# Optimization experiments

Hardware: AMD Instinct MI355X
Metric: run time of the kernel (lower is better)

## Reference

```python
import jax, jax.numpy as jnp
import numpy as np

B, S, D, DH = 4, 2048, 1024, 64


def setup_inputs() -> dict:
    key = jax.random.key(0)
    ks = jax.random.split(key, 7)
    x = jax.random.normal(ks[0], (B, S, D), dtype=jnp.float32)
    def w(k):
        return jax.random.normal(k, (D, DH), dtype=jnp.float32) / np.sqrt(D).astype(np.float32)
    return {
        'x': x,
        'w_q_u': w(ks[1]), 'w_k_u': w(ks[2]), 'w_v_u': w(ks[3]),
        'w_q_c': w(ks[4]), 'w_k_c': w(ks[5]), 'w_v_c': w(ks[6]),
    }


def reference(x, w_q_u, w_k_u, w_v_u, w_q_c, w_k_c, w_v_c):
    b, n, _ = x.shape
    scale = w_q_u.shape[-1] ** -0.5
    # projections (LinearNoBias -> plain matmul)
    Q_u = x @ w_q_u
    K_u = x @ w_k_u
    V_u = x @ w_v_u
    Q_c = x @ w_q_c
    K_c = x @ w_k_c
    V_c = x @ w_v_c

    i = jnp.arange(n)
    causal = i[:, None] >= i[None, :]        # True where j <= i (binary causal / keep for S_c)
    lookahead = i[:, None] < i[None, :]      # True where j > i (allowed in sigmoid term)

    # term1: [b, n, n], zeroed above the diagonal via binary causal mask
    term1 = jnp.einsum('bid,bjd->bij', Q_c, V_u) * scale * causal.astype(x.dtype)

    # sigmoid gate: lookahead mask adds -inf on/below the diagonal -> sigmoid = 0 there
    logits_u = jnp.einsum('bid,bjd->bij', Q_u, K_u) * scale
    sigmoid_term = jax.nn.sigmoid(jnp.where(lookahead, logits_u, -jnp.inf))

    # nested n^3 matmul: S_u[b,i,k] = sum_j term1[b,i,j] * sigmoid_term[b,k,j]
    S_u = jnp.einsum('bij,bkj->bik', term1, sigmoid_term)

    S_c = jnp.where(causal, jnp.einsum('bid,bjd->bij', Q_c, K_c) * scale, -jnp.inf)

    attn = jax.nn.softmax(S_c - jax.nn.silu(S_u), axis=-1)
    return jnp.einsum('bij,bjd->bid', attn, V_c)
```

## Files before the change

### kernel.cpp

```cpp
#include <hip/hip_runtime.h>
#include <hip/hip_bf16.h>

typedef short bf16x8 __attribute__((ext_vector_type(8)));
typedef float f32x4  __attribute__((ext_vector_type(4)));
typedef _Float16 f16x8 __attribute__((ext_vector_type(8)));

#define MFMA16(a,b,c)  __builtin_amdgcn_mfma_f32_16x16x32_bf16((a),(b),(c),0,0,0)
#define MFMAF16(a,b,c) __builtin_amdgcn_mfma_f32_16x16x32_f16((a),(b),(c),0,0,0)

#define GLDS16(g,l) __builtin_amdgcn_global_load_lds( \
    (const __attribute__((address_space(1))) void*)(g), \
    (__attribute__((address_space(3))) void*)(l), 16, 0, 0)

__device__ __forceinline__ short f2bf(float f){
  union { float f; unsigned u; } v; v.f = f;
  unsigned r = v.u + 0x7fffu + ((v.u >> 16) & 1u);
  return (short)(r >> 16);
}
__device__ __forceinline__ float bf2f(short h){
  union { unsigned u; float f; } v; v.u = ((unsigned)(unsigned short)h) << 16;
  return v.f;
}
__device__ __forceinline__ void split8v(f32x4 a, f32x4 b, bf16x8& h, bf16x8& l){
  float t[8] = {a[0],a[1],a[2],a[3],b[0],b[1],b[2],b[3]};
  #pragma unroll
  for (int e = 0; e < 8; ++e){
    short hs = f2bf(t[e]);
    h[e] = hs;
    l[e] = f2bf(t[e] - bf2f(hs));
  }
}

__global__ void k_wt(const float* w0, const float* w1, const float* w2,
                     const float* w3, const float* w4, const float* w5,
                     unsigned short* __restrict__ wth, unsigned short* __restrict__ wtl){
  int p = blockIdx.y;
  const float* wp = p==0?w0:p==1?w1:p==2?w2:p==3?w3:p==4?w4:w5;
  int idx = blockIdx.x*256 + threadIdx.x;
  int n = idx >> 10, k = idx & 1023;
  float v = wp[k*64 + n];
  short hs = f2bf(v);
  wth[(size_t)p*65536 + n*1024 + k] = (unsigned short)hs;
  wtl[(size_t)p*65536 + n*1024 + k] = (unsigned short)f2bf(v - bf2f(hs));
}

__global__ void k_xsplit(const float* __restrict__ x,
                         unsigned short* __restrict__ xh, unsigned short* __restrict__ xl){
  size_t i = ((size_t)blockIdx.x*256 + threadIdx.x)*8;
  f32x4 a = *(const f32x4*)(x + i);
  f32x4 b = *(const f32x4*)(x + i + 4);
  bf16x8 h, l;
  split8v(a, b, h, l);
  *(bf16x8*)(xh + i) = h;
  *(bf16x8*)(xl + i) = l;
}

__global__ __launch_bounds__(256) void k_proj(
    const unsigned short* __restrict__ xh, const unsigned short* __restrict__ xl,
    const unsigned short* __restrict__ wth, const unsigned short* __restrict__ wtl,
    float* __restrict__ proj,
    unsigned short* __restrict__ projh, unsigned short* __restrict__ projl){
  __shared__ __align__(16) char sm[49152];
  int blk = blockIdx.x;
  int rb = blk/3, pg = blk - rb*3;
  int tid = threadIdx.x, w = tid >> 6, lane = tid & 63;
  int lm = lane & 15, quad = lane >> 4;
  int srow = lane >> 3, scg = (lane & 7) ^ srow;
  const char* xhg = (const char*)xh;
  const char* xlg = (const char*)xl;
  const char* w0h = (const char*)wth + (size_t)(pg*2  )*131072;
  const char* w0l = (const char*)wtl + (size_t)(pg*2  )*131072;
  const char* w1h = (const char*)wth + (size_t)(pg*2+1)*131072;
  const char* w1l = (const char*)wtl + (size_t)(pg*2+1)*131072;
  f32x4 acc[2][4] = {};
  for (int k0 = 0; k0 < 1024; k0 += 64){
    __syncthreads();
    size_t cb = (size_t)k0*2 + scg*16;
    #pragma unroll
    for (int i2 = 0; i2 < 2; ++i2){
      int i = w*2 + i2;
      size_t gx = (size_t)(rb*64 + i*8 + srow)*2048 + cb;
      size_t gw = (size_t)(i*8 + srow)*2048 + cb;
      GLDS16(xhg + gx, sm +         i*1024);
      GLDS16(xlg + gx, sm +  8192 + i*1024);
      GLDS16(w0h + gw, sm + 16384 + i*1024);
      GLDS16(w0l + gw, sm + 24576 + i*1024);
      GLDS16(w1h + gw, sm + 32768 + i*1024);
      GLDS16(w1l + gw, sm + 40960 + i*1024);
    }
    __syncthreads();
    #pragma unroll
    for (int ks = 0; ks < 2; ++ks){
      int ra = w*16 + lm;
      int offa = ra*128 + (((ks*4+quad) ^ (ra&7))*16);
      bf16x8 ah = *(const bf16x8*)(sm + offa);
      bf16x8 al = *(const bf16x8*)(sm + 8192 + offa);
      #pragma unroll
      for (int sub = 0; sub < 2; ++sub){
        #pragma unroll
        for (int n = 0; n < 4; ++n){
          int r = n*16 + lm;
          int off = r*128 + (((ks*4+quad) ^ (r&7))*16);
          bf16x8 bh = *(const bf16x8*)(sm + 16384 + sub*16384 + off);
          bf16x8 bl = *(const bf16x8*)(sm + 24576 + sub*16384 + off);
          acc[sub][n] = MFMA16(ah, bh, acc[sub][n]);
          acc[sub][n] = MFMA16(ah, bl, acc[sub][n]);
          acc[sub][n] = MFMA16(al, bh, acc[sub][n]);
        }
      }
    }
  }
  #pragma unroll
  for (int sub = 0; sub < 2; ++sub){
    int p = pg*2 + sub;
    if (p == 2 || p == 5){
      float* op = proj + (size_t)(p == 5 ? 1 : 0)*524288;
      #pragma unroll
      for (int n = 0; n < 4; ++n)
        #pragma unroll
        for (int e = 0; e < 4; ++e){
          int r = rb*64 + w*16 + quad*4 + e;
          op[(size_t)r*64 + n*16 + lm] = acc[sub][n][e];
        }
    }
    if (p != 5){
      unsigned short* oph = projh + (size_t)p*524288;
      unsigned short* opl = projl + (size_t)p*524288;
      #pragma unroll
      for (int n = 0; n < 4; ++n)
        #pragma unroll
        for (int e = 0; e < 4; ++e){
          int r = rb*64 + w*16 + quad*4 + e;
          float f = acc[sub][n][e];
          short hs = f2bf(f);
          oph[(size_t)r*64 + n*16 + lm] = (unsigned short)hs;
          opl[(size_t)r*64 + n*16 + lm] = (unsigned short)f2bf(f - bf2f(hs));
        }
    }
  }
}

__global__ void k_vt(const float* __restrict__ proj, _Float16* __restrict__ vct,
                     _Float16* __restrict__ vuth, _Float16* __restrict__ vutl){
  __shared__ float T[64][65];
  int b = blockIdx.y, stg = blockIdx.x;
  bool isVu = stg >= 32;
  int st = stg & 31;
  int tid = threadIdx.x;
  const float* src = proj + (isVu ? 0 : 524288) + (size_t)b*131072;
  int sloc = tid >> 2, cp = (tid & 3)*16;
  #pragma unroll
  for (int j = 0; j < 4; ++j){
    f32x4 v = *(const f32x4*)(src + (size_t)(st*64 + sloc)*64 + cp + j*4);
    #pragma unroll
    for (int e = 0; e < 4; ++e) T[sloc][cp + j*4 + e] = v[e];
  }
  __syncthreads();
  int d = tid >> 2, sp = (tid & 3)*16;
  size_t o = (size_t)b*131072 + (size_t)d*2048 + st*64 + sp;
  if (!isVu){
    f16x8 h0, h1;
    #pragma unroll
    for (int j = 0; j < 8; ++j) h0[j] = (_Float16)T[sp + j][d];
    #pragma unroll
    for (int j = 0; j < 8; ++j) h1[j] = (_Float16)T[sp + 8 + j][d];
    *(f16x8*)(vct + o) = h0; *(f16x8*)(vct + o + 8) = h1;
  } else {
    f16x8 h0, h1, l0, l1;
    #pragma unroll
    for (int j = 0; j < 8; ++j){
      float f = T[sp + j][d];
      _Float16 h = (_Float16)f;
      h0[j] = h; l0[j] = (_Float16)(f - (float)h);
    }
    #pragma unroll
    for (int j = 0; j < 8; ++j){
      float f = T[sp + 8 + j][d];
      _Float16 h = (_Float16)f;
      h1[j] = h; l1[j] = (_Float16)(f - (float)h);
    }
    *(f16x8*)(vuth + o) = h0; *(f16x8*)(vuth + o + 8) = h1;
    *(f16x8*)(vutl + o) = l0; *(f16x8*)(vutl + o + 8) = l1;
  }
}

__global__ __launch_bounds__(256,2) void k_p2(
    const unsigned short* __restrict__ ph, const unsigned short* __restrict__ pl,
    _Float16* __restrict__ sg, _Float16* __restrict__ t1d){
  __shared__ __align__(16) char sm[65536];
  int b = blockIdx.y;
  int t = blockIdx.x;
  bool isSig = t < 136;
  int a = 0, bb = 0;
  if (isSig){
    #pragma unroll 1
    for (int aa = 0; aa < 16; ++aa){
      int c = 16 - aa;
      if (t < c){ a = aa; bb = aa + t; break; }
      t -= c;
    }
  } else {
    a = bb = t - 136;
  }
  int pa = isSig ? 0 : 3;
  int pb = isSig ? 1 : 2;
  const char* Ahg = (const char*)ph + (size_t)pa*1048576;
  const char* Alg = (const char*)pl + (size_t)pa*1048576;
  const char* Bhg = (const char*)ph + (size_t)pb*1048576;
  const char* Blg = (const char*)pl + (size_t)pb*1048576;
  int tid = threadIdx.x, w = tid >> 6, lane = tid & 63;
  int lm = lane & 15, quad = lane >> 4;
  int srow = lane >> 3, scg = (lane & 7) ^ srow;
  int wm = (w & 1)*64, wn = (w >> 1)*64;
  #pragma unroll
  for (int i2 = 0; i2 < 4; ++i2){
    int i = w*4 + i2;
    int rl = i*8 + srow;
    size_t ga = (size_t)(b*2048 + a*128  + rl)*128 + scg*16;
    size_t gb = (size_t)(b*2048 + bb*128 + rl)*128 + scg*16;
    GLDS16(Ahg + ga, sm +         i*1024);
    GLDS16(Alg + ga, sm + 16384 + i*1024);
    GLDS16(Bhg + gb, sm + 32768 + i*1024);
    GLDS16(Blg + gb, sm + 49152 + i*1024);
  }
  __syncthreads();
  f32x4 acc[4][4] = {};
  #pragma unroll
  for (int ks = 0; ks < 2; ++ks){
    bf16x8 bh[4], bl[4];
    #pragma unroll
    for (int n = 0; n < 4; ++n){
      int r = wn + n*16 + lm;
      int off = r*128 + (((ks*4+quad) ^ (r&7))*16);
      bh[n] = *(const bf16x8*)(sm + 32768 + off);
      bl[n] = *(const bf16x8*)(sm + 49152 + off);
    }
    #pragma unroll
    for (int m = 0; m < 4; ++m){
      int r = wm + m*16 + lm;
      int off = r*128 + (((ks*4+quad) ^ (r&7))*16);
      bf16x8 ah = *(const bf16x8*)(sm + off);
      bf16x8 al = *(const bf16x8*)(sm + 16384 + off);
      #pragma unroll
      for (int n = 0; n < 4; ++n){
        acc[m][n] = MFMA16(ah, bh[n], acc[m][n]);
        acc[m][n] = MFMA16(ah, bl[n], acc[m][n]);
        acc[m][n] = MFMA16(al, bh[n], acc[m][n]);
      }
    }
  }
  __syncthreads();
  _Float16* Tt = (_Float16*)sm;
  #pragma unroll
  for (int m = 0; m < 4; ++m){
    #pragma unroll
    for (int n = 0; n < 4; ++n){
      #pragma unroll
      for (int e = 0; e < 4; ++e){
        int il = wm + m*16 + quad*4 + e;
        int jl = wn + n*16 + lm;
        int gi = a*128 + il, gj = bb*128 + jl;
        float v = acc[m][n][e];
        float outv;
        if (isSig) outv = (gj >  gi) ? (1.0f/(1.0f + __expf(-v*0.125f))) : 0.0f;
        else       outv = (gj <= gi) ? v : 0.0f;
        Tt[il*128 + jl] = (_Float16)outv;
      }
    }
  }
  __syncthreads();
  char* outp = isSig
    ? (char*)(sg + (size_t)b*4194304 + (size_t)(a*128)*2048 + bb*128)
    : (char*)t1d + (size_t)(b*16 + a)*32768;
  size_t rstride = isSig ? 4096 : 256;
  #pragma unroll
  for (int r = 0; r < 8; ++r){
    int lrow = w*32 + r*4 + (lane >> 4);
    int c16 = lane & 15;
    f32x4 vv = *(const f32x4*)(sm + lrow*256 + c16*16);
    *(f32x4*)(outp + (size_t)lrow*rstride + c16*16) = vv;
  }
}

__global__ __launch_bounds__(256) void k_w(
    const _Float16* __restrict__ sg,
    const _Float16* __restrict__ vuth, const _Float16* __restrict__ vutl,
    float* __restrict__ W){
  int p = blockIdx.x, b = blockIdx.y;
  int c = 0, ck = 0;
  #pragma unroll 1
  for (int aa = 0; aa < 16; ++aa){
    if (p < aa + 1){ c = aa; ck = p; break; }
    p -= aa + 1;
  }
  int pidx = blockIdx.x;
  int tid = threadIdx.x, w = tid >> 6, lane = tid & 63;
  int lm = lane & 15, quad = lane >> 4;
  int wm = (w & 1)*64, wn = (w >> 1)*32;
  const char* sgb = (const char*)sg + (size_t)b*8388608;
  f32x4 acc[4][2] = {};
  #pragma unroll
  for (int ks = 0; ks < 4; ++ks){
    f16x8 bh[2], bl[2];
    #pragma unroll
    for (int n = 0; n < 2; ++n){
      int d = wn + n*16 + lm;
      size_t jo = ((size_t)(b*64 + d)*2048 + c*128 + ks*32 + quad*8)*2;
      bh[n] = *(const f16x8*)((const char*)vuth + jo);
      bl[n] = *(const f16x8*)((const char*)vutl + jo);
    }
    #pragma unroll
    for (int m = 0; m < 4; ++m){
      int k = ck*128 + wm + m*16 + lm;
      f16x8 af = *(const f16x8*)(sgb + ((size_t)k*2048 + c*128 + ks*32 + quad*8)*2);
      #pragma unroll
      for (int n = 0; n < 2; ++n){
        acc[m][n] = MFMAF16(af, bh[n], acc[m][n]);
        acc[m][n] = MFMAF16(af, bl[n], acc[m][n]);
      }
    }
  }
  float* Wp = W + (size_t)(b*136 + pidx)*8192;
  #pragma unroll
  for (int m = 0; m < 4; ++m)
    #pragma unroll
    for (int n = 0; n < 2; ++n)
      #pragma unroll
      for (int e = 0; e < 4; ++e){
        int r = wm + m*16 + quad*4 + e;
        int col = wn + n*16 + lm;
        Wp[r*64 + col] = acc[m][n][e];
      }
}

__global__ __launch_bounds__(256) void k_scan(const float* __restrict__ W,
    unsigned short* __restrict__ Ph, unsigned short* __restrict__ Pl){
  int g = blockIdx.x, b = blockIdx.y;
  int ck = g >> 2, ksub = g & 3;
  if (ck >= 15) return;
  int tid = threadIdx.x;
  int rl = ksub*32 + (tid >> 3);
  int col = (tid & 7)*8;
  float acc[8] = {};
  #pragma unroll 1
  for (int c = ck; c < 15; ++c){
    const float* wt = W + (size_t)(b*136 + c*(c+1)/2 + ck)*8192 + rl*64 + col;
    f32x4 v0 = *(const f32x4*)wt;
    f32x4 v1 = *(const f32x4*)(wt + 4);
    #pragma unroll
    for (int e = 0; e < 4; ++e){ acc[e] += v0[e]; acc[4+e] += v1[e]; }
    size_t o = ((size_t)(b*16 + c + 1)*2048 + ck*128 + rl)*64 + col;
    bf16x8 h, l;
    #pragma unroll
    for (int e = 0; e < 8; ++e){
      short hs = f2bf(acc[e]);
      h[e] = hs;
      l[e] = f2bf(acc[e] - bf2f(hs));
    }
    *(bf16x8*)(Ph + o) = h;
    *(bf16x8*)(Pl + o) = l;
  }
}

__global__ __launch_bounds__(256,2) void k_p3(
    const unsigned short* __restrict__ ph, const unsigned short* __restrict__ pl,
    const _Float16* __restrict__ t1d, const _Float16* __restrict__ sg,
    const unsigned short* __restrict__ Ph, const unsigned short* __restrict__ Pl,
    _Float16* __restrict__ lg){
  __shared__ __align__(16) char sm[32768];
  int t = blockIdx.x, b = blockIdx.y;
  int ci = 0, ck = 0;
  #pragma unroll 1
  for (int aa = 0; aa < 16; ++aa){
    if (t < aa + 1){ ci = aa; ck = t; break; }
    t -= aa + 1;
  }
  int tid = threadIdx.x, w = tid >> 6, lane = tid & 63;
  int lm = lane & 15, quad = lane >> 4;
  int wm = (w & 1)*64, wn = (w >> 1)*64;
  f32x4 su[4][4] = {}, sc[4][4] = {};

  const char* Qh = (const char*)ph + (size_t)3*1048576;
  const char* Ql = (const char*)pl + (size_t)3*1048576;
  const char* Kh = (const char*)ph + (size_t)4*1048576;
  const char* Kl = (const char*)pl + (size_t)4*1048576;

  #pragma unroll
  for (int ks = 0; ks < 2; ++ks){
    bf16x8 kh[4], kl[4];
    #pragma unroll
    for (int n = 0; n < 4; ++n){
      size_t off = (size_t)(b*2048 + ck*128 + wn + n*16 + lm)*128 + (ks*32 + quad*8)*2;
      kh[n] = *(const bf16x8*)(Kh + off);
      kl[n] = *(const bf16x8*)(Kl + off);
    }
    #pragma unroll
    for (int m = 0; m < 4; ++m){
      size_t off = (size_t)(b*2048 + ci*128 + wm + m*16 + lm)*128 + (ks*32 + quad*8)*2;
      bf16x8 ah = *(const bf16x8*)(Qh + off);
      bf16x8 al = *(const bf16x8*)(Ql + off);
      #pragma unroll
      for (int n = 0; n < 4; ++n){
        sc[m][n] = MFMA16(ah, kh[n], sc[m][n]);
        sc[m][n] = MFMA16(ah, kl[n], sc[m][n]);
        sc[m][n] = MFMA16(al, kh[n], sc[m][n]);
      }
    }
  }
  if (ck < ci){
    #pragma unroll
    for (int ks = 0; ks < 2; ++ks){
      bf16x8 bh[4], bl[4];
      #pragma unroll
      for (int n = 0; n < 4; ++n){
        size_t off = (((size_t)(b*16 + ci)*2048 + ck*128 + wn + n*16 + lm)*64 + ks*32 + quad*8)*2;
        bh[n] = *(const bf16x8*)((const char*)Ph + off);
        bl[n] = *(const bf16x8*)((const char*)Pl + off);
      }
      #pragma unroll
      for (int m = 0; m < 4; ++m){
        size_t off = (size_t)(b*2048 + ci*128 + wm + m*16 + lm)*128 + (ks*32 + quad*8)*2;
        bf16x8 ah = *(const bf16x8*)(Qh + off);
        bf16x8 al = *(const bf16x8*)(Ql + off);
        #pragma unroll
        for (int n = 0; n < 4; ++n){
          su[m][n] = MFMA16(ah, bh[n], su[m][n]);
          su[m][n] = MFMA16(ah, bl[n], su[m][n]);
          su[m][n] = MFMA16(al, bh[n], su[m][n]);
        }
      }
    }
  }
  const char* t1b = (const char*)t1d + (size_t)(b*16 + ci)*32768;
  const char* sgb = (const char*)sg + (size_t)b*8388608;
  #pragma unroll
  for (int ks = 0; ks < 4; ++ks){
    f16x8 bs[4];
    #pragma unroll
    for (int n = 0; n < 4; ++n)
      bs[n] = *(const f16x8*)(sgb + ((size_t)(ck*128 + wn + n*16 + lm)*2048 + ci*128 + ks*32 + quad*8)*2);
    #pragma unroll
    for (int m = 0; m < 4; ++m){
      f16x8 at = *(const f16x8*)(t1b + ((wm + m*16 + lm)*128 + ks*32 + quad*8)*2);
      #pragma unroll
      for (int n = 0; n < 4; ++n)
        su[m][n] = MFMAF16(at, bs[n], su[m][n]);
    }
  }
  _Float16* Tt = (_Float16*)sm;
  #pragma unroll
  for (int m = 0; m < 4; ++m)
    #pragma unroll
    for (int n = 0; n < 4; ++n)
      #pragma unroll
      for (int e = 0; e < 4; ++e){
        int il = wm + m*16 + quad*4 + e;
        int jl = wn + n*16 + lm;
        float xv = 0.125f*su[m][n][e];
        float sg1 = 1.0f/(1.0f + __expf(-xv));
        Tt[il*128 + jl] = (_Float16)(sc[m][n][e]*0.125f - xv*sg1);
      }
  __syncthreads();
  _Float16* lgb = lg + (size_t)b*4194304;
  #pragma unroll
  for (int r = 0; r < 8; ++r){
    int lrow = w*32 + r*4 + (lane >> 4);
    int c16 = lane & 15;
    f32x4 vv = *(const f32x4*)(sm + lrow*256 + c16*16);
    *(f32x4*)((char*)(lgb + (size_t)(ci*128 + lrow)*2048 + ck*128) + c16*16) = vv;
  }
}

__global__ __launch_bounds__(256,2) void k_p4(const _Float16* __restrict__ lg,
    const _Float16* __restrict__ vct, float* __restrict__ out){
  __shared__ __align__(16) char sm[66048];
  float* Mz = (float*)(sm + 65536);
  float* Sz = (float*)(sm + 65792);
  int b = blockIdx.y;
  int b1 = blockIdx.x;
  int tid = threadIdx.x, w = tid >> 6, lane = tid & 63;
  int lm = lane & 15, quad = lane >> 4;
  const _Float16* vb = vct + (size_t)b*131072;
  for (int pass = 0; pass < 2; ++pass){
    int band = pass ? (127 - b1) : b1;
    int r0 = band*16;
    const char* lgb = (const char*)lg + ((size_t)b*4194304 + (size_t)r0*2048)*2;
    int nkt = ((r0 + 15) >> 6) + 1;
    int fc = (r0 + 1) >> 6;
    int srl = lane >> 3, ssl = lane & 7;
    __syncthreads();
    for (int kt = w; kt < nkt; kt += 4){
      #pragma unroll
      for (int i2 = 0; i2 < 2; ++i2){
        int rl = i2*8 + srl;
        GLDS16(lgb + (size_t)rl*4096 + kt*128 + ((ssl ^ (rl & 7))*16),
               sm + kt*2048 + i2*1024);
      }
    }
    __syncthreads();
    float m_r = -3.0e38f;
    for (int kt = w; kt < nkt; kt += 4){
      #pragma unroll
      for (int half = 0; half < 2; ++half){
        int sl = quad*2 + half;
        f16x8 v = *(const f16x8*)(sm + kt*2048 + lm*128 + ((sl ^ (lm & 7))*16));
        int cb = kt*64 + sl*8;
        #pragma unroll
        for (int e = 0; e < 8; ++e)
          m_r = (cb + e <= r0 + lm) ? fmaxf(m_r, (float)v[e]) : m_r;
      }
    }
    m_r = fmaxf(m_r, __shfl_xor(m_r, 16));
    m_r = fmaxf(m_r, __shfl_xor(m_r, 32));
    Mz[w*16 + lm] = m_r;
    __syncthreads();
    float mfin = fmaxf(fmaxf(Mz[lm], Mz[16 + lm]), fmaxf(Mz[32 + lm], Mz[48 + lm]));
    float s_r = 0.0f;
    for (int kt = w; kt < nkt; kt += 4){
      #pragma unroll
      for (int half = 0; half < 2; ++half){
        int sl = quad*2 + half;
        f16x8 v = *(const f16x8*)(sm + kt*2048 + lm*128 + ((sl ^ (lm & 7))*16));
        int cb = kt*64 + sl*8;
        #pragma unroll
        for (int e = 0; e < 8; ++e)
          if (cb + e <= r0 + lm) s_r += __expf((float)v[e] - mfin);
      }
    }
    s_r += __shfl_xor(s_r, 16);
    s_r += __shfl_xor(s_r, 32);
    Sz[w*16 + lm] = s_r;
    f32x4 acc[4] = {};
    for (int kt = w; kt < nkt; kt += 4){
      bool full = kt < fc;
      #pragma unroll
      for (int ks = 0; ks < 2; ++ks){
        f16x8 Lv = *(const f16x8*)(sm + kt*2048 + lm*128 + (((ks*4+quad) ^ (lm & 7))*16));
        int jbase = kt*64 + ks*32 + quad*8;
        f16x8 af;
        #pragma unroll
        for (int e = 0; e < 8; ++e){
          float p = __expf((float)Lv[e] - mfin);
          if (!full && (jbase + e > r0 + lm)) p = 0.0f;
          af[e] = (_Float16)p;
        }
        #pragma unroll
        for (int n = 0; n < 4; ++n){
          f16x8 bv = *(const f16x8*)(vb + (size_t)(n*16 + lm)*2048 + jbase);
          acc[n] = MFMAF16(af, bv, acc[n]);
        }
      }
    }
    __syncthreads();
    float* Ot = (float*)sm;
    #pragma unroll
    for (int n = 0; n < 4; ++n)
      #pragma unroll
      for (int e = 0; e < 4; ++e)
        Ot[(w*16 + quad*4 + e)*64 + n*16 + lm] = acc[n][e];
    __syncthreads();
    int row = tid >> 4, c4 = (tid & 15)*4;
    f32x4 s = *(const f32x4*)&Ot[row*64 + c4];
    #pragma unroll
    for (int ww = 1; ww < 4; ++ww){
      f32x4 t2 = *(const f32x4*)&Ot[(ww*16 + row)*64 + c4];
      s[0]+=t2[0]; s[1]+=t2[1]; s[2]+=t2[2]; s[3]+=t2[3];
    }
    float z = Sz[row] + Sz[16 + row] + Sz[32 + row] + Sz[48 + row];
    f32x4 o = { s[0]/z, s[1]/z, s[2]/z, s[3]/z };
    *(f32x4*)(out + ((size_t)b*2048 + r0 + row)*64 + c4) = o;
  }
}

static const size_t OFF_PROJ  = 0;
static const size_t OFF_WTH   = 4194304;
static const size_t OFF_WTL   = 4980736;
static const size_t OFF_PROJH = 5767168;
static const size_t OFF_PROJL = 12058624;
static const size_t OFF_VCT   = 18350080;
static const size_t OFF_SG    = 19398656;
static const size_t OFF_LG    = 52953088;
static const size_t OFF_T1D   = 86507520;
static const size_t OFF_PH    = 88604672;
static const size_t OFF_PL    = 105381888;
static const size_t OFF_VUTH  = 122159104;
static const size_t OFF_VUTL  = 123207680;
static const size_t OFF_XH    = 124256256;
static const size_t OFF_XL    = 141033472;
static const size_t OFF_W     = OFF_XH;

extern "C" void kernel_launch(void* const* d_in, const int* in_sizes, int n_in,
                              void* d_out, int out_size, void* d_ws, size_t ws_size,
                              hipStream_t stream){
  (void)in_sizes; (void)n_in; (void)out_size; (void)ws_size;
  const float* x = (const float*)d_in[0];
  char* ws = (char*)d_ws;
  float*          proj  = (float*)(ws + OFF_PROJ);
  unsigned short* wth   = (unsigned short*)(ws + OFF_WTH);
  unsigned short* wtl   = (unsigned short*)(ws + OFF_WTL);
  unsigned short* projh = (unsigned short*)(ws + OFF_PROJH);
  unsigned short* projl = (unsigned short*)(ws + OFF_PROJL);
  _Float16*       vct   = (_Float16*)(ws + OFF_VCT);
  _Float16*       sg    = (_Float16*)(ws + OFF_SG);
  _Float16*       lg    = (_Float16*)(ws + OFF_LG);
  _Float16*       t1d   = (_Float16*)(ws + OFF_T1D);
  unsigned short* Phb   = (unsigned short*)(ws + OFF_PH);
  unsigned short* Plb   = (unsigned short*)(ws + OFF_PL);
  _Float16*       vuth  = (_Float16*)(ws + OFF_VUTH);
  _Float16*       vutl  = (_Float16*)(ws + OFF_VUTL);
  unsigned short* xh    = (unsigned short*)(ws + OFF_XH);
  unsigned short* xl    = (unsigned short*)(ws + OFF_XL);
  float*          Wb    = (float*)(ws + OFF_W);

  k_wt    <<<dim3(256,6),  256, 0, stream>>>((const float*)d_in[1], (const float*)d_in[2],
                                             (const float*)d_in[3], (const float*)d_in[4],
                                             (const float*)d_in[5], (const float*)d_in[6], wth, wtl);
  k_xsplit<<<dim3(4096),   256, 0, stream>>>(x, xh, xl);
  k_proj  <<<dim3(384),    256, 0, stream>>>(xh, xl, wth, wtl, proj, projh, projl);
  k_vt    <<<dim3(64,4),   256, 0, stream>>>(proj, vct, vuth, vutl);
  k_p2    <<<dim3(152,4),  256, 0, stream>>>(projh, projl, sg, t1d);
  k_w     <<<dim3(136,4),  256, 0, stream>>>(sg, vuth, vutl, Wb);
  k_scan  <<<dim3(64,4),   256, 0, stream>>>(Wb, Phb, Plb);
  k_p3    <<<dim3(136,4),  256, 0, stream>>>(projh, projl, t1d, sg, Phb, Plb, lg);
  k_p4    <<<dim3(64,4),   256, 0, stream>>>(lg, vct, (float*)d_out);
}
```

Baseline: 220.0 us.

## Compute softmax row max in logits kernel and fuse sum into PV pass

The logits kernel now computes per-row partial maxima (causally masked on diagonal tiles) and writes them to a small workspace buffer. The softmax/PV kernel reads these partial maxima instead of running its own max pass over LDS. It also accumulates the exponent sum inside the PV loop, dropping the separate sum pass and one barrier. This cuts two full sweeps over the logits tile per row band, at the cost of extra shuffles and stores in the logits kernel and a new cross-kernel dependency. The max is taken over fp32 values while the stored logits are fp16, so they can differ slightly.

```diff
diff --git a/kernel.cpp b/kernel.cpp
--- a/kernel.cpp
+++ b/kernel.cpp
@@ -366,7 +366,7 @@
     const unsigned short* __restrict__ ph, const unsigned short* __restrict__ pl,
     const _Float16* __restrict__ t1d, const _Float16* __restrict__ sg,
     const unsigned short* __restrict__ Ph, const unsigned short* __restrict__ Pl,
-    _Float16* __restrict__ lg){
+    _Float16* __restrict__ lg, float* __restrict__ rmx){
   __shared__ __align__(16) char sm[32768];
   int t = blockIdx.x, b = blockIdx.y;
   int ci = 0, ck = 0;
@@ -448,18 +448,31 @@
     }
   }
   _Float16* Tt = (_Float16*)sm;
-  #pragma unroll
-  for (int m = 0; m < 4; ++m)
-    #pragma unroll
-    for (int n = 0; n < 4; ++n)
-      #pragma unroll
-      for (int e = 0; e < 4; ++e){
-        int il = wm + m*16 + quad*4 + e;
+  bool diag = (ck == ci);
+  #pragma unroll
+  for (int m = 0; m < 4; ++m){
+    #pragma unroll
+    for (int e = 0; e < 4; ++e){
+      int il = wm + m*16 + quad*4 + e;
+      float vmax = -3.0e38f;
+      #pragma unroll
+      for (int n = 0; n < 4; ++n){
         int jl = wn + n*16 + lm;
         float xv = 0.125f*su[m][n][e];
         float sg1 = 1.0f/(1.0f + __expf(-xv));
-        Tt[il*128 + jl] = (_Float16)(sc[m][n][e]*0.125f - xv*sg1);
-      }
+        float val = sc[m][n][e]*0.125f - xv*sg1;
+        Tt[il*128 + jl] = (_Float16)val;
+        bool ok = !diag || (jl <= il);
+        vmax = ok ? fmaxf(vmax, val) : vmax;
+      }
+      vmax = fmaxf(vmax, __shfl_xor(vmax, 1));
+      vmax = fmaxf(vmax, __shfl_xor(vmax, 2));
+      vmax = fmaxf(vmax, __shfl_xor(vmax, 4));
+      vmax = fmaxf(vmax, __shfl_xor(vmax, 8));
+      if (lm == m*4 + e)
+        rmx[((size_t)b*32 + ck*2 + (w >> 1))*2048 + ci*128 + il] = vmax;
+    }
+  }
   __syncthreads();
   _Float16* lgb = lg + (size_t)b*4194304;
   #pragma unroll
@@ -472,10 +485,10 @@
 }
 
 __global__ __launch_bounds__(256,2) void k_p4(const _Float16* __restrict__ lg,
-    const _Float16* __restrict__ vct, float* __restrict__ out){
-  __shared__ __align__(16) char sm[66048];
-  float* Mz = (float*)(sm + 65536);
-  float* Sz = (float*)(sm + 65792);
+    const _Float16* __restrict__ vct, const float* __restrict__ rmx,
+    float* __restrict__ out){
+  __shared__ __align__(16) char sm[65792];
+  float* Sz = (float*)(sm + 65536);
   int b = blockIdx.y;
   int b1 = blockIdx.x;
   int tid = threadIdx.x, w = tid >> 6, lane = tid & 63;
@@ -497,39 +510,15 @@
                sm + kt*2048 + i2*1024);
       }
     }
+    int ci2 = r0 >> 7;
+    float mfin = -3.0e38f;
+    {
+      const float* rp = rmx + (size_t)b*32*2048 + r0 + lm;
+      #pragma unroll 1
+      for (int s = 0; s < 2*(ci2+1); ++s) mfin = fmaxf(mfin, rp[(size_t)s*2048]);
+    }
     __syncthreads();
-    float m_r = -3.0e38f;
-    for (int kt = w; kt < nkt; kt += 4){
-      #pragma unroll
-      for (int half = 0; half < 2; ++half){
-        int sl = quad*2 + half;
-        f16x8 v = *(const f16x8*)(sm + kt*2048 + lm*128 + ((sl ^ (lm & 7))*16));
-        int cb = kt*64 + sl*8;
-        #pragma unroll
-        for (int e = 0; e < 8; ++e)
-          m_r = (cb + e <= r0 + lm) ? fmaxf(m_r, (float)v[e]) : m_r;
-      }
-    }
-    m_r = fmaxf(m_r, __shfl_xor(m_r, 16));
-    m_r = fmaxf(m_r, __shfl_xor(m_r, 32));
-    Mz[w*16 + lm] = m_r;
-    __syncthreads();
-    float mfin = fmaxf(fmaxf(Mz[lm], Mz[16 + lm]), fmaxf(Mz[32 + lm], Mz[48 + lm]));
     float s_r = 0.0f;
-    for (int kt = w; kt < nkt; kt += 4){
-      #pragma unroll
-      for (int half = 0; half < 2; ++half){
-        int sl = quad*2 + half;
-        f16x8 v = *(const f16x8*)(sm + kt*2048 + lm*128 + ((sl ^ (lm & 7))*16));
-        int cb = kt*64 + sl*8;
-        #pragma unroll
-        for (int e = 0; e < 8; ++e)
-          if (cb + e <= r0 + lm) s_r += __expf((float)v[e] - mfin);
-      }
-    }
-    s_r += __shfl_xor(s_r, 16);
-    s_r += __shfl_xor(s_r, 32);
-    Sz[w*16 + lm] = s_r;
     f32x4 acc[4] = {};
     for (int kt = w; kt < nkt; kt += 4){
       bool full = kt < fc;
@@ -542,6 +531,7 @@
         for (int e = 0; e < 8; ++e){
           float p = __expf((float)Lv[e] - mfin);
           if (!full && (jbase + e > r0 + lm)) p = 0.0f;
+          s_r += p;
           af[e] = (_Float16)p;
         }
         #pragma unroll
@@ -551,6 +541,9 @@
         }
       }
     }
+    s_r += __shfl_xor(s_r, 16);
+    s_r += __shfl_xor(s_r, 32);
+    Sz[w*16 + lm] = s_r;
     __syncthreads();
     float* Ot = (float*)sm;
     #pragma unroll
@@ -588,6 +581,7 @@
 static const size_t OFF_XH    = 124256256;
 static const size_t OFF_XL    = 141033472;
 static const size_t OFF_W     = OFF_XH;
+static const size_t OFF_RMX   = 157810688;
 
 extern "C" void kernel_launch(void* const* d_in, const int* in_sizes, int n_in,
                               void* d_out, int out_size, void* d_ws, size_t ws_size,
@@ -611,6 +605,7 @@
   unsigned short* xh    = (unsigned short*)(ws + OFF_XH);
   unsigned short* xl    = (unsigned short*)(ws + OFF_XL);
   float*          Wb    = (float*)(ws + OFF_W);
+  float*          rmx   = (float*)(ws + OFF_RMX);
 
   k_wt    <<<dim3(256,6),  256, 0, stream>>>((const float*)d_in[1], (const float*)d_in[2],
                                              (const float*)d_in[3], (const float*)d_in[4],
@@ -621,6 +616,6 @@
   k_p2    <<<dim3(152,4),  256, 0, stream>>>(projh, projl, sg, t1d);
   k_w     <<<dim3(136,4),  256, 0, stream>>>(sg, vuth, vutl, Wb);
   k_scan  <<<dim3(64,4),   256, 0, stream>>>(Wb, Phb, Plb);
-  k_p3    <<<dim3(136,4),  256, 0, stream>>>(projh, projl, t1d, sg, Phb, Plb, lg);
-  k_p4    <<<dim3(64,4),   256, 0, stream>>>(lg, vct, (float*)d_out);
-}
+  k_p3    <<<dim3(136,4),  256, 0, stream>>>(projh, projl, t1d, sg, Phb, Plb, lg, rmx);
+  k_p4    <<<dim3(64,4),   256, 0, stream>>>(lg, vct, rmx, (float*)d_out);
+}
```

After: 226.8 us. +3.1%, slower.

## Fuse prep kernels, fold V transpose into projection and W into sigmoid kernel

Applied to the files above, without the earlier changes.

Merges weight transpose/split and x split into one launch, moves the V transpose/fp16 split into the projection epilogue (dropping the fp32 proj buffer and k_vt), and computes the W partial products directly from the sigmoid tile held in LDS inside k_p2, eliminating k_w and its re-read of sg from global memory. The LDS tile now uses an XOR swizzle to avoid bank conflicts on the new reads. This cuts three launches and substantial global traffic, at the cost of a longer k_p2 with extra register pressure and LDS-bound work.

```diff
diff --git a/kernel.cpp b/kernel.cpp
--- a/kernel.cpp
+++ b/kernel.cpp
@@ -31,35 +31,37 @@
   }
 }
 
-__global__ void k_wt(const float* w0, const float* w1, const float* w2,
-                     const float* w3, const float* w4, const float* w5,
-                     unsigned short* __restrict__ wth, unsigned short* __restrict__ wtl){
-  int p = blockIdx.y;
-  const float* wp = p==0?w0:p==1?w1:p==2?w2:p==3?w3:p==4?w4:w5;
-  int idx = blockIdx.x*256 + threadIdx.x;
-  int n = idx >> 10, k = idx & 1023;
-  float v = wp[k*64 + n];
-  short hs = f2bf(v);
-  wth[(size_t)p*65536 + n*1024 + k] = (unsigned short)hs;
-  wtl[(size_t)p*65536 + n*1024 + k] = (unsigned short)f2bf(v - bf2f(hs));
-}
-
-__global__ void k_xsplit(const float* __restrict__ x,
-                         unsigned short* __restrict__ xh, unsigned short* __restrict__ xl){
-  size_t i = ((size_t)blockIdx.x*256 + threadIdx.x)*8;
-  f32x4 a = *(const f32x4*)(x + i);
-  f32x4 b = *(const f32x4*)(x + i + 4);
-  bf16x8 h, l;
-  split8v(a, b, h, l);
-  *(bf16x8*)(xh + i) = h;
-  *(bf16x8*)(xl + i) = l;
+__global__ void k_prep(const float* w0, const float* w1, const float* w2,
+                       const float* w3, const float* w4, const float* w5,
+                       const float* __restrict__ x,
+                       unsigned short* __restrict__ wth, unsigned short* __restrict__ wtl,
+                       unsigned short* __restrict__ xh, unsigned short* __restrict__ xl){
+  int gb = blockIdx.x;
+  if (gb < 1536){
+    int p = gb >> 8;
+    const float* wp = p==0?w0:p==1?w1:p==2?w2:p==3?w3:p==4?w4:w5;
+    int idx = (gb & 255)*256 + threadIdx.x;
+    int n = idx >> 10, k = idx & 1023;
+    float v = wp[k*64 + n];
+    short hs = f2bf(v);
+    wth[(size_t)p*65536 + n*1024 + k] = (unsigned short)hs;
+    wtl[(size_t)p*65536 + n*1024 + k] = (unsigned short)f2bf(v - bf2f(hs));
+  } else {
+    size_t i = ((size_t)(gb - 1536)*256 + threadIdx.x)*8;
+    f32x4 a = *(const f32x4*)(x + i);
+    f32x4 b = *(const f32x4*)(x + i + 4);
+    bf16x8 h, l;
+    split8v(a, b, h, l);
+    *(bf16x8*)(xh + i) = h;
+    *(bf16x8*)(xl + i) = l;
+  }
 }
 
 __global__ __launch_bounds__(256) void k_proj(
     const unsigned short* __restrict__ xh, const unsigned short* __restrict__ xl,
     const unsigned short* __restrict__ wth, const unsigned short* __restrict__ wtl,
-    float* __restrict__ proj,
-    unsigned short* __restrict__ projh, unsigned short* __restrict__ projl){
+    unsigned short* __restrict__ projh, unsigned short* __restrict__ projl,
+    _Float16* __restrict__ vct, _Float16* __restrict__ vuth, _Float16* __restrict__ vutl){
   __shared__ __align__(16) char sm[49152];
   int blk = blockIdx.x;
   int rb = blk/3, pg = blk - rb*3;
@@ -113,16 +115,6 @@
   #pragma unroll
   for (int sub = 0; sub < 2; ++sub){
     int p = pg*2 + sub;
-    if (p == 2 || p == 5){
-      float* op = proj + (size_t)(p == 5 ? 1 : 0)*524288;
-      #pragma unroll
-      for (int n = 0; n < 4; ++n)
-        #pragma unroll
-        for (int e = 0; e < 4; ++e){
-          int r = rb*64 + w*16 + quad*4 + e;
-          op[(size_t)r*64 + n*16 + lm] = acc[sub][n][e];
-        }
-    }
     if (p != 5){
       unsigned short* oph = projh + (size_t)p*524288;
       unsigned short* opl = projl + (size_t)p*524288;
@@ -138,55 +130,50 @@
         }
     }
   }
-}
-
-__global__ void k_vt(const float* __restrict__ proj, _Float16* __restrict__ vct,
-                     _Float16* __restrict__ vuth, _Float16* __restrict__ vutl){
-  __shared__ float T[64][65];
-  int b = blockIdx.y, stg = blockIdx.x;
-  bool isVu = stg >= 32;
-  int st = stg & 31;
-  int tid = threadIdx.x;
-  const float* src = proj + (isVu ? 0 : 524288) + (size_t)b*131072;
-  int sloc = tid >> 2, cp = (tid & 3)*16;
-  #pragma unroll
-  for (int j = 0; j < 4; ++j){
-    f32x4 v = *(const f32x4*)(src + (size_t)(st*64 + sloc)*64 + cp + j*4);
-    #pragma unroll
-    for (int e = 0; e < 4; ++e) T[sloc][cp + j*4 + e] = v[e];
-  }
-  __syncthreads();
-  int d = tid >> 2, sp = (tid & 3)*16;
-  size_t o = (size_t)b*131072 + (size_t)d*2048 + st*64 + sp;
-  if (!isVu){
-    f16x8 h0, h1;
-    #pragma unroll
-    for (int j = 0; j < 8; ++j) h0[j] = (_Float16)T[sp + j][d];
-    #pragma unroll
-    for (int j = 0; j < 8; ++j) h1[j] = (_Float16)T[sp + 8 + j][d];
-    *(f16x8*)(vct + o) = h0; *(f16x8*)(vct + o + 8) = h1;
-  } else {
-    f16x8 h0, h1, l0, l1;
-    #pragma unroll
-    for (int j = 0; j < 8; ++j){
-      float f = T[sp + j][d];
-      _Float16 h = (_Float16)f;
-      h0[j] = h; l0[j] = (_Float16)(f - (float)h);
-    }
-    #pragma unroll
-    for (int j = 0; j < 8; ++j){
-      float f = T[sp + 8 + j][d];
-      _Float16 h = (_Float16)f;
-      h1[j] = h; l1[j] = (_Float16)(f - (float)h);
-    }
-    *(f16x8*)(vuth + o) = h0; *(f16x8*)(vuth + o + 8) = h1;
-    *(f16x8*)(vutl + o) = l0; *(f16x8*)(vutl + o + 8) = l1;
+  if (pg == 1 || pg == 2){
+    int sub = (pg == 1) ? 0 : 1;
+    float (*T)[65] = (float (*)[65])sm;
+    __syncthreads();
+    #pragma unroll
+    for (int n = 0; n < 4; ++n)
+      #pragma unroll
+      for (int e = 0; e < 4; ++e)
+        T[w*16 + quad*4 + e][n*16 + lm] = acc[sub][n][e];
+    __syncthreads();
+    int b2 = rb >> 5, sl = (rb & 31)*64;
+    int d = tid >> 2, sp = (tid & 3)*16;
+    size_t o = (size_t)b2*131072 + (size_t)d*2048 + sl + sp;
+    if (sub == 1){
+      f16x8 h0, h1;
+      #pragma unroll
+      for (int j = 0; j < 8; ++j) h0[j] = (_Float16)T[sp + j][d];
+      #pragma unroll
+      for (int j = 0; j < 8; ++j) h1[j] = (_Float16)T[sp + 8 + j][d];
+      *(f16x8*)(vct + o) = h0; *(f16x8*)(vct + o + 8) = h1;
+    } else {
+      f16x8 h0, h1, l0, l1;
+      #pragma unroll
+      for (int j = 0; j < 8; ++j){
+        float f = T[sp + j][d];
+        _Float16 h = (_Float16)f;
+        h0[j] = h; l0[j] = (_Float16)(f - (float)h);
+      }
+      #pragma unroll
+      for (int j = 0; j < 8; ++j){
+        float f = T[sp + 8 + j][d];
+        _Float16 h = (_Float16)f;
+        h1[j] = h; l1[j] = (_Float16)(f - (float)h);
+      }
+      *(f16x8*)(vuth + o) = h0; *(f16x8*)(vuth + o + 8) = h1;
+      *(f16x8*)(vutl + o) = l0; *(f16x8*)(vutl + o + 8) = l1;
+    }
   }
 }
 
 __global__ __launch_bounds__(256,2) void k_p2(
     const unsigned short* __restrict__ ph, const unsigned short* __restrict__ pl,
-    _Float16* __restrict__ sg, _Float16* __restrict__ t1d){
+    const _Float16* __restrict__ vuth, const _Float16* __restrict__ vutl,
+    _Float16* __restrict__ sg, _Float16* __restrict__ t1d, float* __restrict__ W){
   __shared__ __align__(16) char sm[65536];
   int b = blockIdx.y;
   int t = blockIdx.x;
@@ -250,7 +237,6 @@
     }
   }
   __syncthreads();
-  _Float16* Tt = (_Float16*)sm;
   #pragma unroll
   for (int m = 0; m < 4; ++m){
     #pragma unroll
@@ -264,7 +250,7 @@
         float outv;
         if (isSig) outv = (gj >  gi) ? (1.0f/(1.0f + __expf(-v*0.125f))) : 0.0f;
         else       outv = (gj <= gi) ? v : 0.0f;
-        Tt[il*128 + jl] = (_Float16)outv;
+        *(_Float16*)(sm + ((il*256 + jl*2) ^ ((il & 7) << 4))) = (_Float16)outv;
       }
     }
   }
@@ -277,60 +263,45 @@
   for (int r = 0; r < 8; ++r){
     int lrow = w*32 + r*4 + (lane >> 4);
     int c16 = lane & 15;
-    f32x4 vv = *(const f32x4*)(sm + lrow*256 + c16*16);
+    f32x4 vv = *(const f32x4*)(sm + ((lrow*256 + c16*16) ^ ((lrow & 7) << 4)));
     *(f32x4*)(outp + (size_t)lrow*rstride + c16*16) = vv;
   }
-}
-
-__global__ __launch_bounds__(256) void k_w(
-    const _Float16* __restrict__ sg,
-    const _Float16* __restrict__ vuth, const _Float16* __restrict__ vutl,
-    float* __restrict__ W){
-  int p = blockIdx.x, b = blockIdx.y;
-  int c = 0, ck = 0;
-  #pragma unroll 1
-  for (int aa = 0; aa < 16; ++aa){
-    if (p < aa + 1){ c = aa; ck = p; break; }
-    p -= aa + 1;
-  }
-  int pidx = blockIdx.x;
-  int tid = threadIdx.x, w = tid >> 6, lane = tid & 63;
-  int lm = lane & 15, quad = lane >> 4;
-  int wm = (w & 1)*64, wn = (w >> 1)*32;
-  const char* sgb = (const char*)sg + (size_t)b*8388608;
-  f32x4 acc[4][2] = {};
-  #pragma unroll
-  for (int ks = 0; ks < 4; ++ks){
-    f16x8 bh[2], bl[2];
-    #pragma unroll
-    for (int n = 0; n < 2; ++n){
-      int d = wn + n*16 + lm;
-      size_t jo = ((size_t)(b*64 + d)*2048 + c*128 + ks*32 + quad*8)*2;
-      bh[n] = *(const f16x8*)((const char*)vuth + jo);
-      bl[n] = *(const f16x8*)((const char*)vutl + jo);
-    }
-    #pragma unroll
-    for (int m = 0; m < 4; ++m){
-      int k = ck*128 + wm + m*16 + lm;
-      f16x8 af = *(const f16x8*)(sgb + ((size_t)k*2048 + c*128 + ks*32 + quad*8)*2);
+  if (isSig){
+    int wm2 = (w & 1)*64, wn2 = (w >> 1)*32;
+    f32x4 acc2[4][2] = {};
+    #pragma unroll
+    for (int ks = 0; ks < 4; ++ks){
+      f16x8 bh2[2], bl2[2];
       #pragma unroll
       for (int n = 0; n < 2; ++n){
-        acc[m][n] = MFMAF16(af, bh[n], acc[m][n]);
-        acc[m][n] = MFMAF16(af, bl[n], acc[m][n]);
-      }
-    }
-  }
-  float* Wp = W + (size_t)(b*136 + pidx)*8192;
-  #pragma unroll
-  for (int m = 0; m < 4; ++m)
-    #pragma unroll
-    for (int n = 0; n < 2; ++n)
-      #pragma unroll
-      for (int e = 0; e < 4; ++e){
-        int r = wm + m*16 + quad*4 + e;
-        int col = wn + n*16 + lm;
-        Wp[r*64 + col] = acc[m][n][e];
-      }
+        int d = wn2 + n*16 + lm;
+        size_t jo = ((size_t)(b*64 + d)*2048 + bb*128 + ks*32 + quad*8)*2;
+        bh2[n] = *(const f16x8*)((const char*)vuth + jo);
+        bl2[n] = *(const f16x8*)((const char*)vutl + jo);
+      }
+      #pragma unroll
+      for (int m = 0; m < 4; ++m){
+        int k = wm2 + m*16 + lm;
+        f16x8 af = *(const f16x8*)(sm + ((k*256 + ks*64 + quad*16) ^ ((k & 7) << 4)));
+        #pragma unroll
+        for (int n = 0; n < 2; ++n){
+          acc2[m][n] = MFMAF16(af, bh2[n], acc2[m][n]);
+          acc2[m][n] = MFMAF16(af, bl2[n], acc2[m][n]);
+        }
+      }
+    }
+    float* Wp = W + (size_t)(b*136 + bb*(bb+1)/2 + a)*8192;
+    #pragma unroll
+    for (int m = 0; m < 4; ++m)
+      #pragma unroll
+      for (int n = 0; n < 2; ++n)
+        #pragma unroll
+        for (int e = 0; e < 4; ++e){
+          int r = wm2 + m*16 + quad*4 + e;
+          int col = wn2 + n*16 + lm;
+          Wp[r*64 + col] = acc2[m][n][e];
+        }
+  }
 }
 
 __global__ __launch_bounds__(256) void k_scan(const float* __restrict__ W,
@@ -572,7 +543,6 @@
   }
 }
 
-static const size_t OFF_PROJ  = 0;
 static const size_t OFF_WTH   = 4194304;
 static const size_t OFF_WTL   = 4980736;
 static const size_t OFF_PROJH = 5767168;
@@ -595,7 +565,6 @@
   (void)in_sizes; (void)n_in; (void)out_size; (void)ws_size;
   const float* x = (const float*)d_in[0];
   char* ws = (char*)d_ws;
-  float*          proj  = (float*)(ws + OFF_PROJ);
   unsigned short* wth   = (unsigned short*)(ws + OFF_WTH);
   unsigned short* wtl   = (unsigned short*)(ws + OFF_WTL);
   unsigned short* projh = (unsigned short*)(ws + OFF_PROJH);
@@ -612,14 +581,12 @@
   unsigned short* xl    = (unsigned short*)(ws + OFF_XL);
   float*          Wb    = (float*)(ws + OFF_W);
 
-  k_wt    <<<dim3(256,6),  256, 0, stream>>>((const float*)d_in[1], (const float*)d_in[2],
+  k_prep  <<<dim3(5632),   256, 0, stream>>>((const float*)d_in[1], (const float*)d_in[2],
                                              (const float*)d_in[3], (const float*)d_in[4],
-                                             (const float*)d_in[5], (const float*)d_in[6], wth, wtl);
-  k_xsplit<<<dim3(4096),   256, 0, stream>>>(x, xh, xl);
-  k_proj  <<<dim3(384),    256, 0, stream>>>(xh, xl, wth, wtl, proj, projh, projl);
-  k_vt    <<<dim3(64,4),   256, 0, stream>>>(proj, vct, vuth, vutl);
-  k_p2    <<<dim3(152,4),  256, 0, stream>>>(projh, projl, sg, t1d);
-  k_w     <<<dim3(136,4),  256, 0, stream>>>(sg, vuth, vutl, Wb);
+                                             (const float*)d_in[5], (const float*)d_in[6],
+                                             x, wth, wtl, xh, xl);
+  k_proj  <<<dim3(384),    256, 0, stream>>>(xh, xl, wth, wtl, projh, projl, vct, vuth, vutl);
+  k_p2    <<<dim3(152,4),  256, 0, stream>>>(projh, projl, vuth, vutl, sg, t1d, Wb);
   k_scan  <<<dim3(64,4),   256, 0, stream>>>(Wb, Phb, Plb);
   k_p3    <<<dim3(136,4),  256, 0, stream>>>(projh, projl, t1d, sg, Phb, Plb, lg);
   k_p4    <<<dim3(64,4),   256, 0, stream>>>(lg, vct, (float*)d_out);
```

Result: faster. 205.8 us (-6.5%).
